# Kernel tuning notes

Hardware: AMD Instinct MI355X
Metric: run time of the kernel (lower is better)

The kernel has to match this reference:

```python
import jax, jax.numpy as jnp
import numpy as np
import math

B, S, HID = 1, 2048, 1024
NH, NKV = 16, 4
HD = HID // NH          # 64
GROUPS = NH // NKV      # 4
ROPE_BASE = 10000.0


def setup_inputs() -> dict:
    key = jax.random.key(0)
    ks = jax.random.split(key, 5)
    hidden_states = jax.random.normal(ks[0], (B, S, HID), dtype=jnp.float32)
    # additive causal mask: 0 on/below diagonal, -1e9 above
    causal = jnp.triu(jnp.full((S, S), -1e9, dtype=jnp.float32), k=1)
    attention_mask = causal[None, None, :, :]
    position_ids = jnp.arange(S, dtype=jnp.int32)[None, :]
    sc = 0.02
    Wq = jax.random.normal(ks[1], (NH * HD, HID), dtype=jnp.float32) * sc
    Wk = jax.random.normal(ks[2], (NKV * HD, HID), dtype=jnp.float32) * sc
    Wv = jax.random.normal(ks[3], (NKV * HD, HID), dtype=jnp.float32) * sc
    Wo = jax.random.normal(ks[4], (HID, NH * HD), dtype=jnp.float32) * sc
    return {"hidden_states": hidden_states, "attention_mask": attention_mask,
            "position_ids": position_ids, "Wq": Wq, "Wk": Wk, "Wv": Wv, "Wo": Wo}


def _rotate_half(x):
    x1, x2 = jnp.split(x, 2, axis=-1)
    return jnp.concatenate([-x2, x1], axis=-1)


def _rope_cos_sin(position_ids, dtype):
    # LlamaRotaryEmbedding: inv_freq over even dims, emb = [freqs, freqs]
    inv_freq = 1.0 / (ROPE_BASE ** (jnp.arange(0, HD, 2, dtype=jnp.float32) / HD))
    freqs = position_ids.astype(jnp.float32)[..., None] * inv_freq  # [B,S,HD/2]
    emb = jnp.concatenate([freqs, freqs], axis=-1)                  # [B,S,HD]
    return jnp.cos(emb).astype(dtype)[:, None], jnp.sin(emb).astype(dtype)[:, None]


def reference(hidden_states, attention_mask, position_ids, Wq, Wk, Wv, Wo):
    b, q_len, _ = hidden_states.shape
    # torch Linear: y = x @ W.T  (W is [out, in])
    q = jnp.einsum('bsh,oh->bso', hidden_states, Wq).reshape(b, q_len, NH, HD).transpose(0, 2, 1, 3)
    k = jnp.einsum('bsh,oh->bso', hidden_states, Wk).reshape(b, q_len, NKV, HD).transpose(0, 2, 1, 3)
    v = jnp.einsum('bsh,oh->bso', hidden_states, Wv).reshape(b, q_len, NKV, HD).transpose(0, 2, 1, 3)

    cos, sin = _rope_cos_sin(position_ids, q.dtype)  # [B,1,S,HD]
    q = q * cos + _rotate_half(q) * sin
    k = k * cos + _rotate_half(k) * sin

    # repeat_kv (GQA expansion)
    k = jnp.repeat(k, GROUPS, axis=1)  # [B,NH,S,HD]
    v = jnp.repeat(v, GROUPS, axis=1)

    scores = jnp.einsum('bhqd,bhkd->bhqk', q, k) / math.sqrt(HD)
    scores = scores + attention_mask
    attn = jax.nn.softmax(scores.astype(jnp.float32), axis=-1).astype(q.dtype)
    out = jnp.einsum('bhqk,bhkd->bhqd', attn, v)
    out = out.transpose(0, 2, 1, 3).reshape(b, q_len, NH * HD)
    return jnp.einsum('bso,ho->bsh', out, Wo)
```

## Files before the change

### kernel.cpp

```cpp
#include <hip/hip_runtime.h>
#include <hip/hip_bf16.h>
#include <math.h>

#define S_LEN 2048
#define HIDN  1024
#define K_DIM 1024
#define NHEAD 16
#define NKVH  4
#define HD    64

typedef __bf16 bf16x8 __attribute__((ext_vector_type(8)));
typedef float  f32x4  __attribute__((ext_vector_type(4)));
typedef float  f32x16 __attribute__((ext_vector_type(16)));

static __device__ __forceinline__ unsigned short f2bf(float f) {
  union { float f; unsigned u; } v; v.f = f;
  unsigned u = v.u;
  u += 0x7fffu + ((u >> 16) & 1u);
  return (unsigned short)(u >> 16);
}

static __device__ __forceinline__ void gload_lds16(const unsigned short* g, unsigned short* l) {
  __builtin_amdgcn_global_load_lds((const __attribute__((address_space(1))) void*)g,
                                   (__attribute__((address_space(3))) void*)l, 16, 0, 0);
}

__global__ __launch_bounds__(256) void prep_kernel(const float* __restrict__ hs,
                                                   const float* __restrict__ Wq,
                                                   const float* __restrict__ Wk,
                                                   const float* __restrict__ Wv,
                                                   const float* __restrict__ Wo,
                                                   const int* __restrict__ pos,
                                                   unsigned short* __restrict__ hsb,
                                                   unsigned short* __restrict__ Wqkv,
                                                   unsigned short* __restrict__ Wob,
                                                   float2* __restrict__ cstab) {
  const int gid = blockIdx.x * 256 + threadIdx.x;
  if (gid < 1179648) {
    const float* src; unsigned short* dst; int i;
    if (gid < 524288)       { src = hs; dst = hsb;            i = gid; }
    else if (gid < 786432)  { src = Wq; dst = Wqkv;           i = gid - 524288; }
    else if (gid < 851968)  { src = Wk; dst = Wqkv + 1048576; i = gid - 786432; }
    else if (gid < 917504)  { src = Wv; dst = Wqkv + 1310720; i = gid - 851968; }
    else                    { src = Wo; dst = Wob;            i = gid - 917504; }
    float4 v = *(const float4*)(src + (size_t)i * 4);
    ushort4 u;
    u.x = f2bf(v.x); u.y = f2bf(v.y); u.z = f2bf(v.z); u.w = f2bf(v.w);
    *(ushort4*)(dst + (size_t)i * 4) = u;
  } else {
    int e = gid - 1179648;
    int s = e >> 5, ir = e & 31;
    float p = (float)pos[s];
    float ang = p * __expf(-(float)ir * 0.28782314f);
    float c, sn;
    sincosf(ang, &sn, &c);
    cstab[e] = make_float2(c, sn);
  }
}

template <bool ROPE>
__global__ __launch_bounds__(256, 2) void gemm_kernel(const unsigned short* __restrict__ A,
                                                      const unsigned short* __restrict__ B,
                                                      float* __restrict__ C,
                                                      const float2* __restrict__ cstab,
                                                      unsigned short* __restrict__ Qr,
                                                      unsigned short* __restrict__ Kr,
                                                      unsigned short* __restrict__ Vtmp) {
  __shared__ unsigned short As[2][64][64];
  __shared__ unsigned short Bs[2][128][64];
  const int m0 = blockIdx.x * 64, n0 = blockIdx.y * 128;
  const int t = threadIdx.x, w = t >> 6, lane = t & 63;
  const int lr = lane & 15, lg = lane >> 4;
  const int m_off = (w & 1) * 32, n_off = (w >> 1) * 64;
  const int rsub = lane >> 3;
  const int cole = ((lane & 7) * 8) ^ (rsub << 3);
  f32x4 acc[2][4] = {};

#define GSTAGE(b, kt) do {                                                     \
    _Pragma("unroll")                                                          \
    for (int c = 0; c < 2; ++c) {                                              \
      int ch = w * 2 + c;                                                      \
      gload_lds16(A + (size_t)(m0 + ch * 8 + rsub) * K_DIM + (kt) * 64 + cole, \
                  &As[b][0][0] + ch * 512);                                    \
    }                                                                          \
    _Pragma("unroll")                                                          \
    for (int c = 0; c < 4; ++c) {                                              \
      int ch = w * 4 + c;                                                      \
      gload_lds16(B + (size_t)(n0 + ch * 8 + rsub) * K_DIM + (kt) * 64 + cole, \
                  &Bs[b][0][0] + ch * 512);                                    \
    }                                                                          \
  } while (0)

  int cur = 0;
  GSTAGE(0, 0);
  for (int kt = 0; kt < 16; ++kt) {
    __syncthreads();
    if (kt + 1 < 16) GSTAGE(cur ^ 1, kt + 1);
#pragma unroll
    for (int kc = 0; kc < 2; ++kc) {
      bf16x8 af[2], bfg[4];
#pragma unroll
      for (int i = 0; i < 2; ++i) {
        int row = m_off + i * 16 + lr;
        af[i] = *(const bf16x8*)((const char*)&As[cur][0][0] + row * 128 +
                                 ((kc * 64 + lg * 16) ^ ((lr & 7) << 4)));
      }
#pragma unroll
      for (int jj = 0; jj < 4; ++jj) {
        int row = n_off + jj * 16 + lr;
        bfg[jj] = *(const bf16x8*)((const char*)&Bs[cur][0][0] + row * 128 +
                                   ((kc * 64 + lg * 16) ^ ((lr & 7) << 4)));
      }
#pragma unroll
      for (int i = 0; i < 2; ++i)
#pragma unroll
        for (int jj = 0; jj < 4; ++jj)
          acc[i][jj] = __builtin_amdgcn_mfma_f32_16x16x32_bf16(af[i], bfg[jj], acc[i][jj], 0, 0, 0);
    }
    cur ^= 1;
  }

  if constexpr (ROPE) {
    const int col64 = n0 + n_off;
    const int hh = col64 >> 6;
#pragma unroll
    for (int i = 0; i < 2; ++i) {
#pragma unroll
      for (int r = 0; r < 4; ++r) {
        int srow = m0 + m_off + i * 16 + lg * 4 + r;
        if (hh < 20) {
          unsigned short* dst = (hh < 16) ? (Qr + ((size_t)hh * S_LEN + srow) * HD)
                                          : (Kr + ((size_t)(hh - 16) * S_LEN + srow) * HD);
          float sc = (hh < 16) ? 0.125f : 1.0f;
#pragma unroll
          for (int jj = 0; jj < 2; ++jj) {
            int d0 = jj * 16 + lr;
            float2 cs = cstab[(size_t)srow * 32 + d0];
            float v0 = acc[i][jj][r] * sc, v1 = acc[i][jj + 2][r] * sc;
            dst[d0]      = f2bf(v0 * cs.x - v1 * cs.y);
            dst[d0 + 32] = f2bf(v1 * cs.x + v0 * cs.y);
          }
        } else {
          int vcol = col64 - 1280;
#pragma unroll
          for (int jj = 0; jj < 4; ++jj)
            Vtmp[(size_t)srow * 256 + vcol + jj * 16 + lr] = f2bf(acc[i][jj][r]);
        }
      }
    }
  } else {
#pragma unroll
    for (int i = 0; i < 2; ++i)
#pragma unroll
      for (int jj = 0; jj < 4; ++jj)
#pragma unroll
        for (int r = 0; r < 4; ++r)
          C[(size_t)(m0 + m_off + i * 16 + lg * 4 + r) * 1024 + n0 + n_off + jj * 16 + lr] =
              acc[i][jj][r];
  }
}

__global__ __launch_bounds__(256) void transpose_v(const unsigned short* __restrict__ Vtmp,
                                                   unsigned short* __restrict__ Vt) {
  __shared__ unsigned short tile[64][72];
  const int kh = blockIdx.x & 3, st = blockIdx.x >> 2;
  const int s0 = st * 64;
  const int t = threadIdx.x;
  const int r = t >> 3, c = (t & 7) * 8;
#pragma unroll
  for (int p = 0; p < 2; ++p) {
    int row = r + p * 32;
    uint4 v = *(const uint4*)(Vtmp + (size_t)(s0 + row) * 256 + kh * 64 + c);
    *(uint4*)&tile[row][c] = v;
  }
  __syncthreads();
#pragma unroll
  for (int p = 0; p < 2; ++p) {
    int d = r + p * 32;
    int sc = (t & 7) * 8;
    union { unsigned short s[8]; uint4 q; } u;
#pragma unroll
    for (int e = 0; e < 8; ++e) u.s[e] = tile[sc + e][d];
    *(uint4*)(Vt + ((size_t)kh * HD + d) * S_LEN + s0 + sc) = u.q;
  }
}

__global__ __launch_bounds__(256, 4) void attn_part(const unsigned short* __restrict__ Qr,
                                                    const unsigned short* __restrict__ Kr,
                                                    const unsigned short* __restrict__ Vt,
                                                    unsigned short* __restrict__ Ob,
                                                    float* __restrict__ Opart,
                                                    float* __restrict__ Mlpart) {
  __shared__ unsigned short Ks[2][64][64];
  __shared__ unsigned short Vs[2][64][64];
  const int bid = blockIdx.x;
  const int h = bid & 15;
  const int j = bid >> 4;
  int qt, ck;
  if (j < 16)      { qt = 15 - (j >> 2); ck = j & 3; }
  else if (j < 28) { int e = j - 16; int d3 = e / 3; qt = 11 - d3; ck = e - d3 * 3; }
  else if (j < 36) { int e = j - 28; qt = 7 - (e >> 1); ck = e & 1; }
  else             { qt = 39 - j; ck = 0; }
  const int kh = h >> 2;
  const int nkt_all = 2 * qt + 2;
  const int nch = (2 * qt + 9) >> 3;
  const int kt0 = ck * 8;
  const int kt1 = (kt0 + 8 < nkt_all) ? kt0 + 8 : nkt_all;

  const int t = threadIdx.x, w = t >> 6, lane = t & 63;
  const int ql = lane & 31, hi = lane >> 5;
  const int q = qt * 128 + w * 32 + ql;
  const int qwave_max = qt * 128 + w * 32 + 31;

  const unsigned short* Kh = Kr + (size_t)kh * S_LEN * HD;
  const unsigned short* Vh = Vt + (size_t)kh * HD * S_LEN;

  bf16x8 qf[4];
#pragma unroll
  for (int c = 0; c < 4; ++c)
    qf[c] = *(const bf16x8*)(Qr + ((size_t)h * S_LEN + q) * HD + c * 16 + hi * 8);

  const int rsub = lane >> 3;
  const int cole = ((lane & 7) * 8) ^ (rsub << 3);

#define ASTAGE(b, kt) do {                                                           \
    int k0s = (kt) * 64;                                                             \
    _Pragma("unroll")                                                                \
    for (int c = 0; c < 4; ++c) {                                                    \
      int ch = w * 4 + c;                                                            \
      if (ch < 8)                                                                    \
        gload_lds16(Kh + (size_t)(k0s + ch * 8 + rsub) * HD + cole,                  \
                    &Ks[b][0][0] + ch * 512);                                        \
      else                                                                           \
        gload_lds16(Vh + (size_t)((ch - 8) * 8 + rsub) * S_LEN + k0s + cole,         \
                    &Vs[b][0][0] + (ch - 8) * 512);                                  \
    }                                                                                \
  } while (0)

  float m_run = -1e30f, l_run = 0.f;
  f32x16 oacc[2] = {};
  int cur = 0;
  ASTAGE(0, kt0);
  for (int kt = kt0; kt < kt1; ++kt) {
    __syncthreads();
    if (kt + 1 < kt1) ASTAGE(cur ^ 1, kt + 1);
    const int k0 = kt * 64;
    if (k0 <= qwave_max) {
      f32x16 sacc[2] = {};
#pragma unroll
      for (int tt = 0; tt < 2; ++tt)
#pragma unroll
        for (int c = 0; c < 4; ++c) {
          int row = tt * 32 + ql;
          bf16x8 kf = *(const bf16x8*)((const char*)&Ks[cur][0][0] + row * 128 +
                                       ((c * 32 + hi * 16) ^ ((ql & 7) << 4)));
          sacc[tt] = __builtin_amdgcn_mfma_f32_32x32x16_bf16(kf, qf[c], sacc[tt], 0, 0, 0);
        }

      float p[32];
#pragma unroll
      for (int tt = 0; tt < 2; ++tt)
#pragma unroll
        for (int e = 0; e < 16; ++e) p[tt * 16 + e] = sacc[tt][e];

      if (k0 + 63 > q) {
#pragma unroll
        for (int tt = 0; tt < 2; ++tt)
#pragma unroll
          for (int e = 0; e < 16; ++e) {
            int kl = tt * 32 + (e & 3) + 8 * (e >> 2) + 4 * hi;
            if (k0 + kl > q) p[tt * 16 + e] = -1e30f;
          }
      }

      float mx = p[0];
#pragma unroll
      for (int e = 1; e < 32; ++e) mx = fmaxf(mx, p[e]);
      mx = fmaxf(mx, __shfl_xor(mx, 32));

      if (__any(mx > m_run + 8.0f)) {
        float mnew = fmaxf(m_run, mx);
        float f = __expf(m_run - mnew);
        l_run *= f;
        oacc[0] *= f; oacc[1] *= f;
        m_run = mnew;
      }

      float lsum = 0.f;
#pragma unroll
      for (int e = 0; e < 32; ++e) { p[e] = __expf(p[e] - m_run); lsum += p[e]; }
      lsum += __shfl_xor(lsum, 32);
      l_run += lsum;

      unsigned g[16];
#pragma unroll
      for (int i = 0; i < 16; ++i) {
        union { __hip_bfloat162 b; unsigned u; } cv;
        cv.b = __float22bfloat162_rn(make_float2(p[2 * i], p[2 * i + 1]));
        g[i] = cv.u;
      }
#pragma unroll
      for (int b4 = 0; b4 < 16; b4 += 8) {
        asm volatile("v_permlane32_swap_b32 %0, %1" : "+v"(g[b4 + 0]), "+v"(g[b4 + 2]));
        asm volatile("v_permlane32_swap_b32 %0, %1" : "+v"(g[b4 + 1]), "+v"(g[b4 + 3]));
        asm volatile("v_permlane32_swap_b32 %0, %1" : "+v"(g[b4 + 4]), "+v"(g[b4 + 6]));
        asm volatile("v_permlane32_swap_b32 %0, %1" : "+v"(g[b4 + 5]), "+v"(g[b4 + 7]));
      }

#pragma unroll
      for (int s = 0; s < 4; ++s) {
        union { bf16x8 v; unsigned u[4]; } pf;
        pf.u[0] = g[s * 4 + 0]; pf.u[1] = g[s * 4 + 1];
        pf.u[2] = g[s * 4 + 2]; pf.u[3] = g[s * 4 + 3];
#pragma unroll
        for (int dt = 0; dt < 2; ++dt) {
          int row = dt * 32 + ql;
          bf16x8 vf = *(const bf16x8*)((const char*)&Vs[cur][0][0] + row * 128 +
                                       ((s * 32 + hi * 16) ^ ((ql & 7) << 4)));
          oacc[dt] = __builtin_amdgcn_mfma_f32_32x32x16_bf16(vf, pf.v, oacc[dt], 0, 0, 0);
        }
      }
    }
    cur ^= 1;
  }

  if (nch == 1) {
    float inv = 1.f / l_run;
#pragma unroll
    for (int dt = 0; dt < 2; ++dt)
#pragma unroll
      for (int gg = 0; gg < 4; ++gg) {
        ushort4 u;
        u.x = f2bf(oacc[dt][gg * 4 + 0] * inv);
        u.y = f2bf(oacc[dt][gg * 4 + 1] * inv);
        u.z = f2bf(oacc[dt][gg * 4 + 2] * inv);
        u.w = f2bf(oacc[dt][gg * 4 + 3] * inv);
        int d0 = dt * 32 + 8 * gg + 4 * hi;
        *(ushort4*)(Ob + (size_t)q * HIDN + h * HD + d0) = u;
      }
  } else {
    const int slot = (h * 16 + qt) * 4 + ck;
    float* ob = Opart + (size_t)slot * 8192 + t * 32;
#pragma unroll
    for (int dt = 0; dt < 2; ++dt)
#pragma unroll
      for (int gg = 0; gg < 4; ++gg) {
        f32x4 v4;
        v4[0] = oacc[dt][gg * 4 + 0]; v4[1] = oacc[dt][gg * 4 + 1];
        v4[2] = oacc[dt][gg * 4 + 2]; v4[3] = oacc[dt][gg * 4 + 3];
        *(f32x4*)(ob + dt * 16 + gg * 4) = v4;
      }
    if (hi == 0)
      *(float2*)(Mlpart + ((size_t)slot * 128 + w * 32 + ql) * 2) = make_float2(m_run, l_run);
  }
}

__global__ __launch_bounds__(256) void attn_merge(const float* __restrict__ Opart,
                                                  const float* __restrict__ Mlpart,
                                                  unsigned short* __restrict__ Ob) {
  const int h = blockIdx.x & 15, qt = 4 + (blockIdx.x >> 4);
  const int nch = (2 * qt + 9) >> 3;
  const int slotb = (h * 16 + qt) * 4;
  const int t = threadIdx.x;
  const int ql = t & 31, hi = (t >> 5) & 1, w = t >> 6;
  const int q_l = w * 32 + ql;
  const int q = qt * 128 + q_l;

  float mc[4], lc[4], mstar = -1e30f;
#pragma unroll
  for (int c = 0; c < 4; ++c)
    if (c < nch) {
      float2 ml = *(const float2*)(Mlpart + ((size_t)(slotb + c) * 128 + q_l) * 2);
      mc[c] = ml.x; lc[c] = ml.y;
      mstar = fmaxf(mstar, ml.x);
    }
  float wgt[4], lsum = 0.f;
#pragma unroll
  for (int c = 0; c < 4; ++c)
    if (c < nch) { wgt[c] = __expf(mc[c] - mstar); lsum += wgt[c] * lc[c]; }
  const float inv = 1.f / lsum;

#pragma unroll
  for (int g = 0; g < 8; ++g) {
    f32x4 a = {};
#pragma unroll
    for (int c = 0; c < 4; ++c)
      if (c < nch) {
        f32x4 v = *(const f32x4*)(Opart + (size_t)(slotb + c) * 8192 + t * 32 + g * 4);
        a += v * wgt[c];
      }
    int dt = g >> 2, gg = g & 3;
    int d0 = dt * 32 + 8 * gg + 4 * hi;
    ushort4 u;
    u.x = f2bf(a[0] * inv); u.y = f2bf(a[1] * inv);
    u.z = f2bf(a[2] * inv); u.w = f2bf(a[3] * inv);
    *(ushort4*)(Ob + (size_t)q * HIDN + h * HD + d0) = u;
  }
}

extern "C" void kernel_launch(void* const* d_in, const int* in_sizes, int n_in,
                              void* d_out, int out_size, void* d_ws, size_t ws_size,
                              hipStream_t stream) {
  const float* hs = (const float*)d_in[0];
  const int* pos = (const int*)d_in[2];
  const float* Wq = (const float*)d_in[3];
  const float* Wk = (const float*)d_in[4];
  const float* Wv = (const float*)d_in[5];
  const float* Wo = (const float*)d_in[6];
  float* out = (float*)d_out;

  char* ws = (char*)d_ws;
  unsigned short* hsb   = (unsigned short*)(ws);
  unsigned short* Wqkv  = (unsigned short*)(ws + 4194304);
  unsigned short* Wob   = (unsigned short*)(ws + 7340032);
  float2*         cstab = (float2*)(ws + 9437184);
  unsigned short* Qr    = (unsigned short*)(ws + 10485760);
  unsigned short* Kr    = (unsigned short*)(ws + 14680064);
  unsigned short* Vtmp  = (unsigned short*)(ws + 15728640);
  unsigned short* Vt    = (unsigned short*)(ws + 16777216);
  unsigned short* Ob    = (unsigned short*)(ws + 17825792);
  float*          Opart = (float*)(ws + 22020096);
  float*          Mlpart= (float*)(ws + 55574528);

  dim3 blk(256);
  prep_kernel<<<4864, blk, 0, stream>>>(hs, Wq, Wk, Wv, Wo, pos, hsb, Wqkv, Wob, cstab);
  gemm_kernel<true><<<dim3(32, 12), blk, 0, stream>>>(hsb, Wqkv, nullptr, cstab, Qr, Kr, Vtmp);
  transpose_v<<<128, blk, 0, stream>>>(Vtmp, Vt);
  attn_part<<<640, blk, 0, stream>>>(Qr, Kr, Vt, Ob, Opart, Mlpart);
  attn_merge<<<192, blk, 0, stream>>>(Opart, Mlpart, Ob);
  gemm_kernel<false><<<dim3(32, 8), blk, 0, stream>>>(Ob, Wob, out, nullptr, nullptr, nullptr, nullptr);
}
```

Measured before the change: 87.84 us.

## Replace split-KV attention with 64-row query tiles and retile QKV GEMM with 32x32 MFMA

Attention drops the split-K partial/merge scheme and instead launches 512 blocks of 128 threads, each covering 64 query rows and looping over every causal key tile, so the merge kernel and the partial-result buffers go away. The QKV projection GEMM now uses 128x128 tiles with 32x32x16 MFMA and s_setprio around the MFMA groups, with the RoPE epilogue adapted to the new accumulator layout. The goal is to remove the merge launch and the partial-output traffic and to raise MFMA efficiency. The cost is unbalanced causal work per block, since late query tiles run up to 32 key steps, and fewer blocks in the QKV GEMM.

Result: slower. 112.5 us (+28.1%).

```diff
diff --git a/kernel.cpp b/kernel.cpp
--- a/kernel.cpp
+++ b/kernel.cpp
@@ -58,14 +58,91 @@
   }
 }
 
-template <bool ROPE>
-__global__ __launch_bounds__(256, 2) void gemm_kernel(const unsigned short* __restrict__ A,
-                                                      const unsigned short* __restrict__ B,
-                                                      float* __restrict__ C,
-                                                      const float2* __restrict__ cstab,
-                                                      unsigned short* __restrict__ Qr,
-                                                      unsigned short* __restrict__ Kr,
-                                                      unsigned short* __restrict__ Vtmp) {
+__global__ __launch_bounds__(256, 2) void gemm_qkv(const unsigned short* __restrict__ A,
+                                                   const unsigned short* __restrict__ B,
+                                                   const float2* __restrict__ cstab,
+                                                   unsigned short* __restrict__ Qr,
+                                                   unsigned short* __restrict__ Kr,
+                                                   unsigned short* __restrict__ Vtmp) {
+  __shared__ unsigned short As[2][128][64];
+  __shared__ unsigned short Bs[2][128][64];
+  const int m0 = blockIdx.x * 128, n0 = blockIdx.y * 128;
+  const int t = threadIdx.x, w = t >> 6, lane = t & 63;
+  const int ql = lane & 31, hi = lane >> 5;
+  const int m_off = (w & 1) * 64, n_off = (w >> 1) * 64;
+  const int rsub = lane >> 3;
+  const int cole = ((lane & 7) * 8) ^ (rsub << 3);
+  f32x16 acc[2][2] = {};
+
+#define QSTAGE(b, kt) do {                                                       \
+    _Pragma("unroll")                                                            \
+    for (int c = 0; c < 4; ++c) {                                                \
+      int ch = w * 4 + c;                                                        \
+      gload_lds16(A + (size_t)(m0 + ch * 8 + rsub) * K_DIM + (kt) * 64 + cole,   \
+                  &As[b][0][0] + ch * 512);                                      \
+      gload_lds16(B + (size_t)(n0 + ch * 8 + rsub) * K_DIM + (kt) * 64 + cole,   \
+                  &Bs[b][0][0] + ch * 512);                                      \
+    }                                                                            \
+  } while (0)
+
+  int cur = 0;
+  QSTAGE(0, 0);
+  for (int kt = 0; kt < 16; ++kt) {
+    __syncthreads();
+    if (kt + 1 < 16) QSTAGE(cur ^ 1, kt + 1);
+#pragma unroll
+    for (int ks = 0; ks < 4; ++ks) {
+      bf16x8 af[2], bfj[2];
+#pragma unroll
+      for (int i = 0; i < 2; ++i) {
+        int row = m_off + i * 32 + ql;
+        af[i] = *(const bf16x8*)((const char*)&As[cur][0][0] + row * 128 +
+                                 ((ks * 32 + hi * 16) ^ ((row & 7) << 4)));
+      }
+#pragma unroll
+      for (int j = 0; j < 2; ++j) {
+        int row = n_off + j * 32 + ql;
+        bfj[j] = *(const bf16x8*)((const char*)&Bs[cur][0][0] + row * 128 +
+                                  ((ks * 32 + hi * 16) ^ ((row & 7) << 4)));
+      }
+      __builtin_amdgcn_s_setprio(1);
+#pragma unroll
+      for (int i = 0; i < 2; ++i)
+#pragma unroll
+        for (int j = 0; j < 2; ++j)
+          acc[i][j] = __builtin_amdgcn_mfma_f32_32x32x16_bf16(af[i], bfj[j], acc[i][j], 0, 0, 0);
+      __builtin_amdgcn_s_setprio(0);
+    }
+    cur ^= 1;
+  }
+
+  const int hh = (n0 + n_off) >> 6;
+#pragma unroll
+  for (int i = 0; i < 2; ++i) {
+#pragma unroll
+    for (int e = 0; e < 16; ++e) {
+      int srow = m0 + m_off + i * 32 + (e & 3) + 8 * (e >> 2) + 4 * hi;
+      float v0 = acc[i][0][e], v1 = acc[i][1][e];
+      if (hh < 20) {
+        unsigned short* dst = (hh < 16) ? (Qr + ((size_t)hh * S_LEN + srow) * HD)
+                                        : (Kr + ((size_t)(hh - 16) * S_LEN + srow) * HD);
+        float sc = (hh < 16) ? 0.125f : 1.0f;
+        float2 cs = cstab[(size_t)srow * 32 + ql];
+        v0 *= sc; v1 *= sc;
+        dst[ql]      = f2bf(v0 * cs.x - v1 * cs.y);
+        dst[ql + 32] = f2bf(v1 * cs.x + v0 * cs.y);
+      } else {
+        int vcol = (n0 + n_off) - 1280;
+        Vtmp[(size_t)srow * 256 + vcol + ql]      = f2bf(v0);
+        Vtmp[(size_t)srow * 256 + vcol + 32 + ql] = f2bf(v1);
+      }
+    }
+  }
+}
+
+__global__ __launch_bounds__(256, 2) void gemm_o(const unsigned short* __restrict__ A,
+                                                 const unsigned short* __restrict__ B,
+                                                 float* __restrict__ C) {
   __shared__ unsigned short As[2][64][64];
   __shared__ unsigned short Bs[2][128][64];
   const int m0 = blockIdx.x * 64, n0 = blockIdx.y * 128;
@@ -76,7 +153,7 @@
   const int cole = ((lane & 7) * 8) ^ (rsub << 3);
   f32x4 acc[2][4] = {};
 
-#define GSTAGE(b, kt) do {                                                     \
+#define OSTAGE(b, kt) do {                                                     \
     _Pragma("unroll")                                                          \
     for (int c = 0; c < 2; ++c) {                                              \
       int ch = w * 2 + c;                                                      \
@@ -92,10 +169,10 @@
   } while (0)
 
   int cur = 0;
-  GSTAGE(0, 0);
+  OSTAGE(0, 0);
   for (int kt = 0; kt < 16; ++kt) {
     __syncthreads();
-    if (kt + 1 < 16) GSTAGE(cur ^ 1, kt + 1);
+    if (kt + 1 < 16) OSTAGE(cur ^ 1, kt + 1);
 #pragma unroll
     for (int kc = 0; kc < 2; ++kc) {
       bf16x8 af[2], bfg[4];
@@ -119,45 +196,14 @@
     }
     cur ^= 1;
   }
-
-  if constexpr (ROPE) {
-    const int col64 = n0 + n_off;
-    const int hh = col64 >> 6;
-#pragma unroll
-    for (int i = 0; i < 2; ++i) {
-#pragma unroll
-      for (int r = 0; r < 4; ++r) {
-        int srow = m0 + m_off + i * 16 + lg * 4 + r;
-        if (hh < 20) {
-          unsigned short* dst = (hh < 16) ? (Qr + ((size_t)hh * S_LEN + srow) * HD)
-                                          : (Kr + ((size_t)(hh - 16) * S_LEN + srow) * HD);
-          float sc = (hh < 16) ? 0.125f : 1.0f;
-#pragma unroll
-          for (int jj = 0; jj < 2; ++jj) {
-            int d0 = jj * 16 + lr;
-            float2 cs = cstab[(size_t)srow * 32 + d0];
-            float v0 = acc[i][jj][r] * sc, v1 = acc[i][jj + 2][r] * sc;
-            dst[d0]      = f2bf(v0 * cs.x - v1 * cs.y);
-            dst[d0 + 32] = f2bf(v1 * cs.x + v0 * cs.y);
-          }
-        } else {
-          int vcol = col64 - 1280;
-#pragma unroll
-          for (int jj = 0; jj < 4; ++jj)
-            Vtmp[(size_t)srow * 256 + vcol + jj * 16 + lr] = f2bf(acc[i][jj][r]);
-        }
-      }
-    }
-  } else {
-#pragma unroll
-    for (int i = 0; i < 2; ++i)
-#pragma unroll
-      for (int jj = 0; jj < 4; ++jj)
-#pragma unroll
-        for (int r = 0; r < 4; ++r)
-          C[(size_t)(m0 + m_off + i * 16 + lg * 4 + r) * 1024 + n0 + n_off + jj * 16 + lr] =
-              acc[i][jj][r];
-  }
+#pragma unroll
+  for (int i = 0; i < 2; ++i)
+#pragma unroll
+    for (int jj = 0; jj < 4; ++jj)
+#pragma unroll
+      for (int r = 0; r < 4; ++r)
+        C[(size_t)(m0 + m_off + i * 16 + lg * 4 + r) * 1024 + n0 + n_off + jj * 16 + lr] =
+            acc[i][jj][r];
 }
 
 __global__ __launch_bounds__(256) void transpose_v(const unsigned short* __restrict__ Vtmp,
@@ -185,32 +231,20 @@
   }
 }
 
-__global__ __launch_bounds__(256, 4) void attn_part(const unsigned short* __restrict__ Qr,
-                                                    const unsigned short* __restrict__ Kr,
-                                                    const unsigned short* __restrict__ Vt,
-                                                    unsigned short* __restrict__ Ob,
-                                                    float* __restrict__ Opart,
-                                                    float* __restrict__ Mlpart) {
+__global__ __launch_bounds__(128, 1) void attn64(const unsigned short* __restrict__ Qr,
+                                                 const unsigned short* __restrict__ Kr,
+                                                 const unsigned short* __restrict__ Vt,
+                                                 unsigned short* __restrict__ Ob) {
   __shared__ unsigned short Ks[2][64][64];
   __shared__ unsigned short Vs[2][64][64];
   const int bid = blockIdx.x;
   const int h = bid & 15;
-  const int j = bid >> 4;
-  int qt, ck;
-  if (j < 16)      { qt = 15 - (j >> 2); ck = j & 3; }
-  else if (j < 28) { int e = j - 16; int d3 = e / 3; qt = 11 - d3; ck = e - d3 * 3; }
-  else if (j < 36) { int e = j - 28; qt = 7 - (e >> 1); ck = e & 1; }
-  else             { qt = 39 - j; ck = 0; }
+  const int qt = 31 - (bid >> 4);
   const int kh = h >> 2;
-  const int nkt_all = 2 * qt + 2;
-  const int nch = (2 * qt + 9) >> 3;
-  const int kt0 = ck * 8;
-  const int kt1 = (kt0 + 8 < nkt_all) ? kt0 + 8 : nkt_all;
-
   const int t = threadIdx.x, w = t >> 6, lane = t & 63;
   const int ql = lane & 31, hi = lane >> 5;
-  const int q = qt * 128 + w * 32 + ql;
-  const int qwave_max = qt * 128 + w * 32 + 31;
+  const int q = qt * 64 + w * 32 + ql;
+  const int nkt = qt + 1;
 
   const unsigned short* Kh = Kr + (size_t)kh * S_LEN * HD;
   const unsigned short* Vh = Vt + (size_t)kh * HD * S_LEN;
@@ -223,179 +257,121 @@
   const int rsub = lane >> 3;
   const int cole = ((lane & 7) * 8) ^ (rsub << 3);
 
-#define ASTAGE(b, kt) do {                                                           \
-    int k0s = (kt) * 64;                                                             \
-    _Pragma("unroll")                                                                \
-    for (int c = 0; c < 4; ++c) {                                                    \
-      int ch = w * 4 + c;                                                            \
-      if (ch < 8)                                                                    \
-        gload_lds16(Kh + (size_t)(k0s + ch * 8 + rsub) * HD + cole,                  \
-                    &Ks[b][0][0] + ch * 512);                                        \
-      else                                                                           \
-        gload_lds16(Vh + (size_t)((ch - 8) * 8 + rsub) * S_LEN + k0s + cole,         \
-                    &Vs[b][0][0] + (ch - 8) * 512);                                  \
-    }                                                                                \
+#define ASTAGE(b, kt) do {                                                        \
+    int k0s = (kt) * 64;                                                          \
+    _Pragma("unroll")                                                             \
+    for (int c = 0; c < 4; ++c) {                                                 \
+      int ch = w * 4 + c;                                                         \
+      gload_lds16(Kh + (size_t)(k0s + ch * 8 + rsub) * HD + cole,                 \
+                  &Ks[b][0][0] + ch * 512);                                       \
+      gload_lds16(Vh + (size_t)(ch * 8 + rsub) * S_LEN + k0s + cole,              \
+                  &Vs[b][0][0] + ch * 512);                                       \
+    }                                                                             \
   } while (0)
 
   float m_run = -1e30f, l_run = 0.f;
   f32x16 oacc[2] = {};
   int cur = 0;
-  ASTAGE(0, kt0);
-  for (int kt = kt0; kt < kt1; ++kt) {
+  ASTAGE(0, 0);
+  for (int kt = 0; kt < nkt; ++kt) {
     __syncthreads();
-    if (kt + 1 < kt1) ASTAGE(cur ^ 1, kt + 1);
+    if (kt + 1 < nkt) ASTAGE(cur ^ 1, kt + 1);
     const int k0 = kt * 64;
-    if (k0 <= qwave_max) {
-      f32x16 sacc[2] = {};
+
+    f32x16 sacc[2] = {};
+    __builtin_amdgcn_s_setprio(1);
+#pragma unroll
+    for (int tt = 0; tt < 2; ++tt)
+#pragma unroll
+      for (int c = 0; c < 4; ++c) {
+        int row = tt * 32 + ql;
+        bf16x8 kf = *(const bf16x8*)((const char*)&Ks[cur][0][0] + row * 128 +
+                                     ((c * 32 + hi * 16) ^ ((ql & 7) << 4)));
+        sacc[tt] = __builtin_amdgcn_mfma_f32_32x32x16_bf16(kf, qf[c], sacc[tt], 0, 0, 0);
+      }
+    __builtin_amdgcn_s_setprio(0);
+
+    float p[32];
+#pragma unroll
+    for (int tt = 0; tt < 2; ++tt)
+#pragma unroll
+      for (int e = 0; e < 16; ++e) p[tt * 16 + e] = sacc[tt][e];
+
+    if (k0 + 63 > q) {
 #pragma unroll
       for (int tt = 0; tt < 2; ++tt)
 #pragma unroll
-        for (int c = 0; c < 4; ++c) {
-          int row = tt * 32 + ql;
-          bf16x8 kf = *(const bf16x8*)((const char*)&Ks[cur][0][0] + row * 128 +
-                                       ((c * 32 + hi * 16) ^ ((ql & 7) << 4)));
-          sacc[tt] = __builtin_amdgcn_mfma_f32_32x32x16_bf16(kf, qf[c], sacc[tt], 0, 0, 0);
+        for (int e = 0; e < 16; ++e) {
+          int kl = tt * 32 + (e & 3) + 8 * (e >> 2) + 4 * hi;
+          if (k0 + kl > q) p[tt * 16 + e] = -1e30f;
         }
-
-      float p[32];
-#pragma unroll
-      for (int tt = 0; tt < 2; ++tt)
-#pragma unroll
-        for (int e = 0; e < 16; ++e) p[tt * 16 + e] = sacc[tt][e];
-
-      if (k0 + 63 > q) {
-#pragma unroll
-        for (int tt = 0; tt < 2; ++tt)
-#pragma unroll
-          for (int e = 0; e < 16; ++e) {
-            int kl = tt * 32 + (e & 3) + 8 * (e >> 2) + 4 * hi;
-            if (k0 + kl > q) p[tt * 16 + e] = -1e30f;
-          }
-      }
-
-      float mx = p[0];
-#pragma unroll
-      for (int e = 1; e < 32; ++e) mx = fmaxf(mx, p[e]);
-      mx = fmaxf(mx, __shfl_xor(mx, 32));
-
-      if (__any(mx > m_run + 8.0f)) {
-        float mnew = fmaxf(m_run, mx);
-        float f = __expf(m_run - mnew);
-        l_run *= f;
-        oacc[0] *= f; oacc[1] *= f;
-        m_run = mnew;
-      }
-
-      float lsum = 0.f;
-#pragma unroll
-      for (int e = 0; e < 32; ++e) { p[e] = __expf(p[e] - m_run); lsum += p[e]; }
-      lsum += __shfl_xor(lsum, 32);
-      l_run += lsum;
-
-      unsigned g[16];
-#pragma unroll
-      for (int i = 0; i < 16; ++i) {
-        union { __hip_bfloat162 b; unsigned u; } cv;
-        cv.b = __float22bfloat162_rn(make_float2(p[2 * i], p[2 * i + 1]));
-        g[i] = cv.u;
-      }
-#pragma unroll
-      for (int b4 = 0; b4 < 16; b4 += 8) {
-        asm volatile("v_permlane32_swap_b32 %0, %1" : "+v"(g[b4 + 0]), "+v"(g[b4 + 2]));
-        asm volatile("v_permlane32_swap_b32 %0, %1" : "+v"(g[b4 + 1]), "+v"(g[b4 + 3]));
-        asm volatile("v_permlane32_swap_b32 %0, %1" : "+v"(g[b4 + 4]), "+v"(g[b4 + 6]));
-        asm volatile("v_permlane32_swap_b32 %0, %1" : "+v"(g[b4 + 5]), "+v"(g[b4 + 7]));
-      }
-
-#pragma unroll
-      for (int s = 0; s < 4; ++s) {
-        union { bf16x8 v; unsigned u[4]; } pf;
-        pf.u[0] = g[s * 4 + 0]; pf.u[1] = g[s * 4 + 1];
-        pf.u[2] = g[s * 4 + 2]; pf.u[3] = g[s * 4 + 3];
-#pragma unroll
-        for (int dt = 0; dt < 2; ++dt) {
-          int row = dt * 32 + ql;
-          bf16x8 vf = *(const bf16x8*)((const char*)&Vs[cur][0][0] + row * 128 +
-                                       ((s * 32 + hi * 16) ^ ((ql & 7) << 4)));
-          oacc[dt] = __builtin_amdgcn_mfma_f32_32x32x16_bf16(vf, pf.v, oacc[dt], 0, 0, 0);
-        }
-      }
+    }
+
+    float mx = p[0];
+#pragma unroll
+    for (int e = 1; e < 32; ++e) mx = fmaxf(mx, p[e]);
+    mx = fmaxf(mx, __shfl_xor(mx, 32));
+
+    if (__any(mx > m_run + 8.0f)) {
+      float mnew = fmaxf(m_run, mx);
+      float f = __expf(m_run - mnew);
+      l_run *= f;
+      oacc[0] *= f; oacc[1] *= f;
+      m_run = mnew;
+    }
+
+    float lsum = 0.f;
+#pragma unroll
+    for (int e = 0; e < 32; ++e) { p[e] = __expf(p[e] - m_run); lsum += p[e]; }
+    lsum += __shfl_xor(lsum, 32);
+    l_run += lsum;
+
+    unsigned g[16];
+#pragma unroll
+    for (int i = 0; i < 16; ++i) {
+      union { __hip_bfloat162 b; unsigned u; } cv;
+      cv.b = __float22bfloat162_rn(make_float2(p[2 * i], p[2 * i + 1]));
+      g[i] = cv.u;
+    }
+#pragma unroll
+    for (int b4 = 0; b4 < 16; b4 += 8) {
+      asm volatile("v_permlane32_swap_b32 %0, %1" : "+v"(g[b4 + 0]), "+v"(g[b4 + 2]));
+      asm volatile("v_permlane32_swap_b32 %0, %1" : "+v"(g[b4 + 1]), "+v"(g[b4 + 3]));
+      asm volatile("v_permlane32_swap_b32 %0, %1" : "+v"(g[b4 + 4]), "+v"(g[b4 + 6]));
+      asm volatile("v_permlane32_swap_b32 %0, %1" : "+v"(g[b4 + 5]), "+v"(g[b4 + 7]));
+    }
+
+#pragma unroll
+    for (int s = 0; s < 4; ++s) {
+      union { bf16x8 v; unsigned u[4]; } pf;
+      pf.u[0] = g[s * 4 + 0]; pf.u[1] = g[s * 4 + 1];
+      pf.u[2] = g[s * 4 + 2]; pf.u[3] = g[s * 4 + 3];
+      __builtin_amdgcn_s_setprio(1);
+#pragma unroll
+      for (int dt = 0; dt < 2; ++dt) {
+        int row = dt * 32 + ql;
+        bf16x8 vf = *(const bf16x8*)((const char*)&Vs[cur][0][0] + row * 128 +
+                                     ((s * 32 + hi * 16) ^ ((ql & 7) << 4)));
+        oacc[dt] = __builtin_amdgcn_mfma_f32_32x32x16_bf16(vf, pf.v, oacc[dt], 0, 0, 0);
+      }
+      __builtin_amdgcn_s_setprio(0);
     }
     cur ^= 1;
   }
 
-  if (nch == 1) {
-    float inv = 1.f / l_run;
-#pragma unroll
-    for (int dt = 0; dt < 2; ++dt)
-#pragma unroll
-      for (int gg = 0; gg < 4; ++gg) {
-        ushort4 u;
-        u.x = f2bf(oacc[dt][gg * 4 + 0] * inv);
-        u.y = f2bf(oacc[dt][gg * 4 + 1] * inv);
-        u.z = f2bf(oacc[dt][gg * 4 + 2] * inv);
-        u.w = f2bf(oacc[dt][gg * 4 + 3] * inv);
-        int d0 = dt * 32 + 8 * gg + 4 * hi;
-        *(ushort4*)(Ob + (size_t)q * HIDN + h * HD + d0) = u;
-      }
-  } else {
-    const int slot = (h * 16 + qt) * 4 + ck;
-    float* ob = Opart + (size_t)slot * 8192 + t * 32;
-#pragma unroll
-    for (int dt = 0; dt < 2; ++dt)
-#pragma unroll
-      for (int gg = 0; gg < 4; ++gg) {
-        f32x4 v4;
-        v4[0] = oacc[dt][gg * 4 + 0]; v4[1] = oacc[dt][gg * 4 + 1];
-        v4[2] = oacc[dt][gg * 4 + 2]; v4[3] = oacc[dt][gg * 4 + 3];
-        *(f32x4*)(ob + dt * 16 + gg * 4) = v4;
-      }
-    if (hi == 0)
-      *(float2*)(Mlpart + ((size_t)slot * 128 + w * 32 + ql) * 2) = make_float2(m_run, l_run);
-  }
-}
-
-__global__ __launch_bounds__(256) void attn_merge(const float* __restrict__ Opart,
-                                                  const float* __restrict__ Mlpart,
-                                                  unsigned short* __restrict__ Ob) {
-  const int h = blockIdx.x & 15, qt = 4 + (blockIdx.x >> 4);
-  const int nch = (2 * qt + 9) >> 3;
-  const int slotb = (h * 16 + qt) * 4;
-  const int t = threadIdx.x;
-  const int ql = t & 31, hi = (t >> 5) & 1, w = t >> 6;
-  const int q_l = w * 32 + ql;
-  const int q = qt * 128 + q_l;
-
-  float mc[4], lc[4], mstar = -1e30f;
-#pragma unroll
-  for (int c = 0; c < 4; ++c)
-    if (c < nch) {
-      float2 ml = *(const float2*)(Mlpart + ((size_t)(slotb + c) * 128 + q_l) * 2);
-      mc[c] = ml.x; lc[c] = ml.y;
-      mstar = fmaxf(mstar, ml.x);
-    }
-  float wgt[4], lsum = 0.f;
-#pragma unroll
-  for (int c = 0; c < 4; ++c)
-    if (c < nch) { wgt[c] = __expf(mc[c] - mstar); lsum += wgt[c] * lc[c]; }
-  const float inv = 1.f / lsum;
-
-#pragma unroll
-  for (int g = 0; g < 8; ++g) {
-    f32x4 a = {};
-#pragma unroll
-    for (int c = 0; c < 4; ++c)
-      if (c < nch) {
-        f32x4 v = *(const f32x4*)(Opart + (size_t)(slotb + c) * 8192 + t * 32 + g * 4);
-        a += v * wgt[c];
-      }
-    int dt = g >> 2, gg = g & 3;
-    int d0 = dt * 32 + 8 * gg + 4 * hi;
-    ushort4 u;
-    u.x = f2bf(a[0] * inv); u.y = f2bf(a[1] * inv);
-    u.z = f2bf(a[2] * inv); u.w = f2bf(a[3] * inv);
-    *(ushort4*)(Ob + (size_t)q * HIDN + h * HD + d0) = u;
-  }
+  float inv = 1.f / l_run;
+#pragma unroll
+  for (int dt = 0; dt < 2; ++dt)
+#pragma unroll
+    for (int gg = 0; gg < 4; ++gg) {
+      ushort4 u;
+      u.x = f2bf(oacc[dt][gg * 4 + 0] * inv);
+      u.y = f2bf(oacc[dt][gg * 4 + 1] * inv);
+      u.z = f2bf(oacc[dt][gg * 4 + 2] * inv);
+      u.w = f2bf(oacc[dt][gg * 4 + 3] * inv);
+      int d0 = dt * 32 + 8 * gg + 4 * hi;
+      *(ushort4*)(Ob + (size_t)q * HIDN + h * HD + d0) = u;
+    }
 }
 
 extern "C" void kernel_launch(void* const* d_in, const int* in_sizes, int n_in,
@@ -419,14 +395,11 @@
   unsigned short* Vtmp  = (unsigned short*)(ws + 15728640);
   unsigned short* Vt    = (unsigned short*)(ws + 16777216);
   unsigned short* Ob    = (unsigned short*)(ws + 17825792);
-  float*          Opart = (float*)(ws + 22020096);
-  float*          Mlpart= (float*)(ws + 55574528);
 
   dim3 blk(256);
   prep_kernel<<<4864, blk, 0, stream>>>(hs, Wq, Wk, Wv, Wo, pos, hsb, Wqkv, Wob, cstab);
-  gemm_kernel<true><<<dim3(32, 12), blk, 0, stream>>>(hsb, Wqkv, nullptr, cstab, Qr, Kr, Vtmp);
+  gemm_qkv<<<dim3(16, 12), blk, 0, stream>>>(hsb, Wqkv, cstab, Qr, Kr, Vtmp);
   transpose_v<<<128, blk, 0, stream>>>(Vtmp, Vt);
-  attn_part<<<640, blk, 0, stream>>>(Qr, Kr, Vt, Ob, Opart, Mlpart);
-  attn_merge<<<192, blk, 0, stream>>>(Opart, Mlpart, Ob);
-  gemm_kernel<false><<<dim3(32, 8), blk, 0, stream>>>(Ob, Wob, out, nullptr, nullptr, nullptr, nullptr);
-}
+  attn64<<<512, dim3(128), 0, stream>>>(Qr, Kr, Vt, Ob);
+  gemm_o<<<dim3(32, 8), blk, 0, stream>>>(Ob, Wob, out);
+}
```
